# Kernel optimization log

Hardware: AMD Instinct MI355X
Metric: run time of the kernel (lower is better)

## Reference

```python
import jax, jax.numpy as jnp
import numpy as np

N_QUBITS = 14
N_TROTTER = 10
EVO_TIME = 1.0
BATCH = 2048
DIM = 2 ** N_QUBITS

# (-1)**bit_q(idx) for every basis index (Qiskit little-endian: qubit q <-> bit q)
_bits = (np.arange(DIM)[:, None] >> np.arange(N_QUBITS)[None, :]) & 1
_SIGNS = np.asarray(1 - 2 * _bits, dtype=np.float32)  # (DIM, n)


def _apply_1q(psi, U, q, n):
    A = 2 ** (n - 1 - q)
    B = 2 ** q
    psi = psi.reshape(A, 2, B)
    psi = jnp.einsum('ij,ajb->aib', U, psi)
    return psi.reshape(-1)


def _apply_zz(psi, theta, q, n):
    # CX(q,q+1); RZ(theta) on q+1; CX(q,q+1)  ==  diagonal exp(-i*theta/2 * Z_q Z_{q+1})
    A = 2 ** (n - 2 - q)
    B = 2 ** q
    em = jnp.exp(-0.5j * theta)
    ep = jnp.exp(0.5j * theta)
    diag = jnp.stack([em, ep, ep, em])  # axis index = 2*bit_{q+1} + bit_q
    psi = psi.reshape(A, 4, B) * diag[None, :, None]
    return psi.reshape(-1)


def _base_state(J, g):
    # Fixed part of the circuit (same for every sample): H on all qubits, then Trotter steps.
    n = N_QUBITS
    dt = EVO_TIME / N_TROTTER
    inv = 1.0 / np.sqrt(2.0)
    H = jnp.array([[inv, inv], [inv, -inv]], dtype=jnp.complex64)
    psi = jnp.zeros(DIM, dtype=jnp.complex64).at[0].set(1.0)
    for q in range(n):
        psi = _apply_1q(psi, H, q, n)
    for _ in range(N_TROTTER):
        for i in range(n - 1):
            psi = _apply_zz(psi, J[i] * dt, i, n)
        for i in range(n):
            half = 0.5 * g[i] * dt
            c = jnp.cos(half).astype(jnp.complex64)
            ms = -1j * jnp.sin(half)
            RX = jnp.stack([jnp.stack([c, ms]), jnp.stack([ms, c])])
            psi = _apply_1q(psi, RX, i, n)
    return psi


def _expectations(psi):
    # psi: (batch, DIM). Original observable order: block i -> qubit n-1-i, [X, Y, Z].
    n = N_QUBITS
    outs = []
    for i in range(n):
        q = n - 1 - i
        A = 2 ** (n - 1 - q)
        B = 2 ** q
        pr = psi.reshape(-1, A, 2, B)
        p0 = pr[:, :, 0, :]
        p1 = pr[:, :, 1, :]
        c = jnp.sum(jnp.conj(p0) * p1, axis=(1, 2))
        outs.append(2.0 * jnp.real(c))  # <X_q>
        outs.append(2.0 * jnp.imag(c))  # <Y_q>
        outs.append(jnp.sum(p0.real ** 2 + p0.imag ** 2 - p1.real ** 2 - p1.imag ** 2, axis=(1, 2)))  # <Z_q>
    return jnp.stack(outs, axis=1).astype(jnp.float32)


def setup_inputs() -> dict:
    key = jax.random.key(0)
    kx, kj, kg = jax.random.split(key, 3)
    x = jax.random.normal(kx, (BATCH, N_QUBITS), dtype=jnp.float32)
    J = jax.random.uniform(kj, (N_QUBITS - 1,), minval=0.5, maxval=1.5, dtype=jnp.float32)
    g = jax.random.uniform(kg, (N_QUBITS,), minval=0.5, maxval=1.5, dtype=jnp.float32)
    return {"x": x, "J": J, "g": g}


def reference(x, J, g):
    psi0 = _base_state(J, g)  # (DIM,), shared across the batch
    S = jnp.asarray(_SIGNS)   # (DIM, n)
    # Final per-sample RZ(x[b,q]) on qubit q -> diagonal phase exp(-i/2 * sum_q x_q * (-1)^bit_q)
    phase = jnp.exp((-0.5j) * (x @ S.T).astype(jnp.complex64))  # (batch, DIM)
    psi = psi0[None, :] * phase
    return _expectations(psi)
```

## Files before the change

kernel.cpp:

```cpp
#include <hip/hip_runtime.h>

#define NQ     14
#define DIMQ   16384
#define NWG    16
#define NTHR   256

typedef float vfloat4 __attribute__((ext_vector_type(4)));

struct Smem {
    float2 slab[1024];
    float2 tabLo[64];
    float2 tabHi[128];
    float  red[48];
};


__device__ __forceinline__ void ld8v(const float2* p, float rb, float2 r[4]) {
    vfloat4 a, b;
    for (;;) {
        asm volatile("global_load_dwordx4 %0, %2, off sc0 sc1\n\t"
                     "global_load_dwordx4 %1, %2, off offset:16 sc0 sc1\n\t"
                     "s_waitcnt vmcnt(0)"
                     : "=&v"(a), "=&v"(b) : "v"(p) : "memory");
        float m0 = fminf(fminf(a.x * rb, a.y * rb), fminf(a.z * rb, a.w * rb));
        float m1 = fminf(fminf(b.x * rb, b.y * rb), fminf(b.z * rb, b.w * rb));
        bool ok = fminf(m0, m1) > 8.0f;
        if (__ballot(!ok) == 0ull) break;
        __builtin_amdgcn_s_sleep(1);
    }
    r[0] = make_float2(a.x - rb, a.y - rb); r[1] = make_float2(a.z - rb, a.w - rb);
    r[2] = make_float2(b.x - rb, b.y - rb); r[3] = make_float2(b.z - rb, b.w - rb);
}
__device__ __forceinline__ float2 d2f2(double d) { union { double d; float2 f; } u; u.d = d; return u.f; }
__device__ __forceinline__ double f22d(float2 f) { union { double d; float2 f; } u; u.f = f; return u.d; }
__device__ __forceinline__ void st2b(float2* p, float2 v, float wb) {
    float2 e = make_float2(v.x + wb, v.y + wb);
    asm volatile("global_store_dwordx2 %0, %1, off sc0 sc1"
                 : : "v"(p), "v"(f22d(e)) : "memory");
}
__device__ __forceinline__ void st8b(float2* p, const float2 r[4], float wb) {
    vfloat4 a, b;
    a.x = r[0].x + wb; a.y = r[0].y + wb; a.z = r[1].x + wb; a.w = r[1].y + wb;
    b.x = r[2].x + wb; b.y = r[2].y + wb; b.z = r[3].x + wb; b.w = r[3].y + wb;
    asm volatile("global_store_dwordx4 %0, %1, off sc0 sc1\n\t"
                 "global_store_dwordx4 %0, %2, off offset:16 sc0 sc1"
                 : : "v"(p), "v"(a), "v"(b) : "memory");
}
__device__ __forceinline__ void stfb(float* p, float v, float wb) {
    float e = v + wb;
    asm volatile("global_store_dword %0, %1, off sc0 sc1" : : "v"(p), "v"(e) : "memory");
}
__device__ __forceinline__ void ld3v(const float* p, float rb, bool use2,
                                     float& r0, float& r1, float& r2) {
    for (;;) {
        asm volatile("global_load_dword %0, %3, off sc0 sc1\n\t"
                     "global_load_dword %1, %3, off offset:1024 sc0 sc1\n\t"
                     "global_load_dword %2, %3, off offset:2048 sc0 sc1\n\t"
                     "s_waitcnt vmcnt(0)"
                     : "=&v"(r0), "=&v"(r1), "=&v"(r2) : "v"(p) : "memory");
        float m = fminf(r0 * rb, r1 * rb);
        if (use2) m = fminf(m, r2 * rb);
        bool ok = m > 8.0f;
        if (__ballot(!ok) == 0ull) break;
        __builtin_amdgcn_s_sleep(1);
    }
    r0 -= rb; r1 -= rb; r2 -= rb;
}

__device__ __forceinline__ float2 cmulf(float2 a, float2 b) {
    return make_float2(a.x * b.x - a.y * b.y, a.x * b.y + a.y * b.x);
}
__device__ __forceinline__ void bfly(float2& p0, float2& p1, float c, float s) {
    float2 n0 = make_float2(c * p0.x + s * p1.y, c * p0.y - s * p1.x);
    float2 n1 = make_float2(c * p1.x + s * p0.y, c * p1.y - s * p0.x);
    p0 = n0; p1 = n1;
}
__device__ __forceinline__ void bfly_shfl(float2& p, int mask, float c, float s) {
    float qx = __shfl_xor(p.x, mask);
    float qy = __shfl_xor(p.y, mask);
    p = make_float2(c * p.x + s * qy, c * p.y - s * qx);
}
__device__ __forceinline__ void zz_apply(const Smem& sm, float2& a, int k) {
    int d = (k ^ (k >> 1)) & 0x1FFF;
    float2 rot = cmulf(sm.tabLo[d & 63], sm.tabHi[d >> 6]);
    a = cmulf(a, rot);
}
__device__ __forceinline__ void stage_12(float2* slab, float2 r[4], int t) {
    __syncthreads();
#pragma unroll
    for (int j = 0; j < 4; ++j) slab[(t << 2) | j] = r[j];
    __syncthreads();
#pragma unroll
    for (int j = 0; j < 4; ++j) r[j] = slab[t | (j << 8)];
}
__device__ __forceinline__ void stage_21(float2* slab, float2 r[4], int t) {
    __syncthreads();
#pragma unroll
    for (int j = 0; j < 4; ++j) slab[t | (j << 8)] = r[j];
    __syncthreads();
#pragma unroll
    for (int j = 0; j < 4; ++j) r[j] = slab[(t << 2) | j];
}
__device__ __forceinline__ void reduce_qubit(Smem& sm, int sb, int i, int t) {
    float cr = 0.f, ci = 0.f, z = 0.f;
#pragma unroll
    for (int j = 0; j < 4; ++j) {
        const int m = (t << 2) | j;
        const float2 a = sm.slab[m];
        const float n = a.x * a.x + a.y * a.y;
        if ((m >> sb) & 1) {
            z -= n;
        } else {
            z += n;
            const float2 b = sm.slab[m ^ (1 << sb)];
            cr += a.x * b.x + a.y * b.y;
            ci += a.x * b.y - a.y * b.x;
        }
    }
#pragma unroll
    for (int off = 32; off; off >>= 1) {
        cr += __shfl_down(cr, off);
        ci += __shfl_down(ci, off);
        z  += __shfl_down(z, off);
    }
    if ((t & 63) == 0) {
        atomicAdd(&sm.red[3 * i + 0], cr);
        atomicAdd(&sm.red[3 * i + 1], ci);
        atomicAdd(&sm.red[3 * i + 2], z);
    }
}

template <bool FIRST>
__device__ void phaseA(Smem& sm, float2* psi, int w, int t,
                       const float* c, const float* s, float rb, float wb) {
    float2 r[4];
    if (FIRST) {
#pragma unroll
        for (int j = 0; j < 4; ++j) r[j] = make_float2(0.0078125f, 0.0f);
    } else {
        ld8v(&psi[(w << 10) | (t << 2)], rb, r);
#pragma unroll
        for (int b = 2; b < 6; ++b) {
#pragma unroll
            for (int j = 0; j < 4; ++j) bfly_shfl(r[j], 1 << b, c[2 + b], s[2 + b]);
        }
    }
#pragma unroll
    for (int j = 0; j < 4; ++j) zz_apply(sm, r[j], (w << 10) | (t << 2) | j);
    bfly(r[0], r[1], c[0], s[0]); bfly(r[2], r[3], c[0], s[0]);
    bfly(r[0], r[2], c[1], s[1]); bfly(r[1], r[3], c[1], s[1]);
#pragma unroll
    for (int b = 0; b < 6; ++b) {
#pragma unroll
        for (int j = 0; j < 4; ++j) bfly_shfl(r[j], 1 << b, c[2 + b], s[2 + b]);
    }
    stage_12(sm.slab, r, t);
    bfly(r[0], r[1], c[8], s[8]); bfly(r[2], r[3], c[8], s[8]);
    bfly(r[0], r[2], c[9], s[9]); bfly(r[1], r[3], c[9], s[9]);
#pragma unroll
    for (int j = 0; j < 4; ++j) st2b(&psi[(w << 10) | t | (j << 8)], r[j], wb);
}

template <bool KEEPSLAB>
__device__ void phaseB(Smem& sm, float2* psi, int w, int t,
                       const float* c, const float* s, float rb, float wb) {
    float2 r[4];
    const int kbase = ((t >> 2) << 8) | (w << 4) | ((t & 3) << 2);
    ld8v(&psi[kbase], rb, r);
#pragma unroll
    for (int j = 0; j < 4; ++j) bfly_shfl(r[j], 16, c[10], s[10]);
#pragma unroll
    for (int j = 0; j < 4; ++j) bfly_shfl(r[j], 32, c[11], s[11]);
    stage_12(sm.slab, r, t);
    bfly(r[0], r[1], c[12], s[12]); bfly(r[2], r[3], c[12], s[12]);
    bfly(r[0], r[2], c[13], s[13]); bfly(r[1], r[3], c[13], s[13]);
#pragma unroll
    for (int j = 0; j < 4; ++j) {
        const int m = t | (j << 8);
        zz_apply(sm, r[j], ((m >> 4) << 8) | (w << 4) | (m & 15));
    }
    bfly(r[0], r[1], c[12], s[12]); bfly(r[2], r[3], c[12], s[12]);
    bfly(r[0], r[2], c[13], s[13]); bfly(r[1], r[3], c[13], s[13]);
#pragma unroll
    for (int b = 0; b < 4; ++b) {
#pragma unroll
        for (int j = 0; j < 4; ++j) bfly_shfl(r[j], 1 << b, c[b], s[b]);
    }
#pragma unroll
    for (int j = 0; j < 4; ++j) bfly_shfl(r[j], 16, c[8], s[8]);
#pragma unroll
    for (int j = 0; j < 4; ++j) bfly_shfl(r[j], 32, c[9], s[9]);
    stage_21(sm.slab, r, t);
#pragma unroll
    for (int j = 0; j < 4; ++j) bfly_shfl(r[j], 16, c[10], s[10]);
#pragma unroll
    for (int j = 0; j < 4; ++j) bfly_shfl(r[j], 32, c[11], s[11]);
    st8b(&psi[kbase], r, wb);
    if (KEEPSLAB) {
#pragma unroll
        for (int j = 0; j < 4; ++j) sm.slab[(t << 2) | j] = r[j];
    }
}

extern "C" __global__ void __launch_bounds__(NTHR)
qr_all(const float* __restrict__ x, const float* __restrict__ J,
       const float* __restrict__ g, float* __restrict__ out,
       float2* __restrict__ psi, float* __restrict__ P) {
    __shared__ Smem sm;
    const int w = blockIdx.x;
    const int t = threadIdx.x;
    const float dt = 0.1f;

    if (t < 64) {
        float phi = 0.0f;
        for (int i = 0; i < 6; ++i) {
            const float h = 0.5f * J[i] * dt;
            phi += ((t >> i) & 1) ? h : -h;
        }
        float sn, cs; __sincosf(phi, &sn, &cs);
        sm.tabLo[t] = make_float2(cs, sn);
    } else if (t < 192) {
        const int v = t - 64;
        float phi = 0.0f;
        for (int i = 0; i < 7; ++i) {
            const float h = 0.5f * J[6 + i] * dt;
            phi += ((v >> i) & 1) ? h : -h;
        }
        float sn, cs; __sincosf(phi, &sn, &cs);
        sm.tabHi[v] = make_float2(cs, sn);
    }
    if (t < 48) sm.red[t] = 0.0f;
    float cc[NQ], ss[NQ];
#pragma unroll
    for (int i = 0; i < NQ; ++i) __sincosf(0.5f * g[i] * dt, &ss[i], &cc[i]);
    __syncthreads();

    phaseA<true>(sm, psi, w, t, cc, ss, 0.0f, -4.0f);

    float esn[7], ecs[7];
#pragma unroll
    for (int k = 0; k < 7; ++k) {
        const int task = w * NTHR + t + (k << 12);
        const int b = task / NQ;
        const int i = task - b * NQ;
        __sincosf(x[b * NQ + 13 - i], &esn[k], &ecs[k]);
    }

    for (int sstep = 1; sstep <= 9; ++sstep) {
        const float wb = ((sstep + 1) & 1) ? -4.0f : 4.0f;
        const float rb = -wb;
        if (sstep & 1) {
            if (sstep == 9) {
                phaseB<true>(sm, psi, w, t, cc, ss, rb, wb);
                __syncthreads();
#pragma unroll
                for (int q = 0; q <= 3; ++q) reduce_qubit(sm, q, 13 - q, t);
#pragma unroll
                for (int q = 8; q <= 13; ++q) reduce_qubit(sm, q - 4, 13 - q, t);
            } else {
                phaseB<false>(sm, psi, w, t, cc, ss, rb, wb);
            }
        } else {
            phaseA<false>(sm, psi, w, t, cc, ss, rb, wb);
        }
    }

    {
        float2 r[4];
        ld8v(&psi[(w << 10) | (t << 2)], 4.0f, r);
#pragma unroll
        for (int b = 2; b < 6; ++b) {
#pragma unroll
            for (int j = 0; j < 4; ++j) bfly_shfl(r[j], 1 << b, cc[2 + b], ss[2 + b]);
        }
        __syncthreads();
#pragma unroll
        for (int j = 0; j < 4; ++j) sm.slab[(t << 2) | j] = r[j];
        __syncthreads();
#pragma unroll
        for (int q = 4; q <= 7; ++q) reduce_qubit(sm, q, 13 - q, t);
        __syncthreads();
        if (t < 42) stfb(&P[t * NWG + w], sm.red[t], -4.0f);
    }

    float* sumbuf = (float*)sm.slab;
    {
        float r0, r1, r2;
        ld3v(&P[t], -4.0f, t < 160, r0, r1, r2);
        sumbuf[t] = r0; sumbuf[t + 256] = r1; sumbuf[t + 512] = r2;
    }
    __syncthreads();
    float cv = 0.0f;
    if (t < 42) {
#pragma unroll
        for (int k = 0; k < NWG; ++k) cv += sumbuf[t * NWG + k];
    }
    __syncthreads();
    if (t < 42) sm.red[t] = cv;
    __syncthreads();

#pragma unroll
    for (int k = 0; k < 7; ++k) {
        const int task = w * NTHR + t + (k << 12);
        const int b = task / NQ;
        const int i = task - b * NQ;
        const float cr = sm.red[3 * i + 0];
        const float ci = sm.red[3 * i + 1];
        const float zz = sm.red[3 * i + 2];
        const float sn = esn[k], cs = ecs[k];
        float* o = out + b * (3 * NQ) + 3 * i;
        o[0] = 2.0f * (cs * cr - sn * ci);
        o[1] = 2.0f * (sn * cr + cs * ci);
        o[2] = zz;
    }
}

extern "C" void kernel_launch(void* const* d_in, const int* in_sizes, int n_in,
                              void* d_out, int out_size, void* d_ws, size_t ws_size,
                              hipStream_t stream) {
    const float* x = (const float*)d_in[0];
    const float* J = (const float*)d_in[1];
    const float* g = (const float*)d_in[2];
    float* out = (float*)d_out;
    char* ws   = (char*)d_ws;
    float2* psi = (float2*)ws;
    float*  P   = (float*)(ws + DIMQ * sizeof(float2));
    (void)in_sizes; (void)n_in; (void)out_size; (void)ws_size;

    hipLaunchKernelGGL(qr_all, dim3(NWG), dim3(NTHR), 0, stream,
                       x, J, g, out, psi, P);
}
```

Measured before the change: 93.81 us.

## Split state across 64 single-wave workgroups, drop LDS transposes

Changes the launch from 16 workgroups of 256 threads to 64 workgroups of one wavefront each. Each wave now holds 256 amplitudes, so all in-phase butterflies run on registers and cross-lane shuffles, with no LDS slab staging or __syncthreads. Partial expectation values are reduced per wave and written to a workspace with sentinel-biased values. Every wave then polls all 64 partial sets and reduces them by shuffles. This removes LDS round trips and block barriers, at the cost of more workgroups polling global memory at each phase boundary and a larger final gather.

```diff
diff --git a/kernel.cpp b/kernel.cpp
--- a/kernel.cpp
+++ b/kernel.cpp
@@ -1,19 +1,17 @@
 #include <hip/hip_runtime.h>
 
-#define NQ     14
-#define DIMQ   16384
-#define NWG    16
-#define NTHR   256
+#define NQ    14
+#define DIMQ  16384
+#define NWG   64
+#define NTHR  64
 
 typedef float vfloat4 __attribute__((ext_vector_type(4)));
 
 struct Smem {
-    float2 slab[1024];
     float2 tabLo[64];
     float2 tabHi[128];
     float  red[48];
 };
-
 
 __device__ __forceinline__ void ld8v(const float2* p, float rb, float2 r[4]) {
     vfloat4 a, b;
@@ -31,13 +29,6 @@
     r[0] = make_float2(a.x - rb, a.y - rb); r[1] = make_float2(a.z - rb, a.w - rb);
     r[2] = make_float2(b.x - rb, b.y - rb); r[3] = make_float2(b.z - rb, b.w - rb);
 }
-__device__ __forceinline__ float2 d2f2(double d) { union { double d; float2 f; } u; u.d = d; return u.f; }
-__device__ __forceinline__ double f22d(float2 f) { union { double d; float2 f; } u; u.f = f; return u.d; }
-__device__ __forceinline__ void st2b(float2* p, float2 v, float wb) {
-    float2 e = make_float2(v.x + wb, v.y + wb);
-    asm volatile("global_store_dwordx2 %0, %1, off sc0 sc1"
-                 : : "v"(p), "v"(f22d(e)) : "memory");
-}
 __device__ __forceinline__ void st8b(float2* p, const float2 r[4], float wb) {
     vfloat4 a, b;
     a.x = r[0].x + wb; a.y = r[0].y + wb; a.z = r[1].x + wb; a.w = r[1].y + wb;
@@ -50,21 +41,35 @@
     float e = v + wb;
     asm volatile("global_store_dword %0, %1, off sc0 sc1" : : "v"(p), "v"(e) : "memory");
 }
-__device__ __forceinline__ void ld3v(const float* p, float rb, bool use2,
-                                     float& r0, float& r1, float& r2) {
+__device__ __forceinline__ void ld48v(const float* p, vfloat4 v[12]) {
     for (;;) {
-        asm volatile("global_load_dword %0, %3, off sc0 sc1\n\t"
-                     "global_load_dword %1, %3, off offset:1024 sc0 sc1\n\t"
-                     "global_load_dword %2, %3, off offset:2048 sc0 sc1\n\t"
-                     "s_waitcnt vmcnt(0)"
-                     : "=&v"(r0), "=&v"(r1), "=&v"(r2) : "v"(p) : "memory");
-        float m = fminf(r0 * rb, r1 * rb);
-        if (use2) m = fminf(m, r2 * rb);
-        bool ok = m > 8.0f;
+        asm volatile(
+            "global_load_dwordx4 %0,  %12, off sc0 sc1\n\t"
+            "global_load_dwordx4 %1,  %12, off offset:16 sc0 sc1\n\t"
+            "global_load_dwordx4 %2,  %12, off offset:32 sc0 sc1\n\t"
+            "global_load_dwordx4 %3,  %12, off offset:48 sc0 sc1\n\t"
+            "global_load_dwordx4 %4,  %12, off offset:64 sc0 sc1\n\t"
+            "global_load_dwordx4 %5,  %12, off offset:80 sc0 sc1\n\t"
+            "global_load_dwordx4 %6,  %12, off offset:96 sc0 sc1\n\t"
+            "global_load_dwordx4 %7,  %12, off offset:112 sc0 sc1\n\t"
+            "global_load_dwordx4 %8,  %12, off offset:128 sc0 sc1\n\t"
+            "global_load_dwordx4 %9,  %12, off offset:144 sc0 sc1\n\t"
+            "global_load_dwordx4 %10, %12, off offset:160 sc0 sc1\n\t"
+            "global_load_dwordx4 %11, %12, off offset:176 sc0 sc1\n\t"
+            "s_waitcnt vmcnt(0)"
+            : "=&v"(v[0]), "=&v"(v[1]), "=&v"(v[2]), "=&v"(v[3]),
+              "=&v"(v[4]), "=&v"(v[5]), "=&v"(v[6]), "=&v"(v[7]),
+              "=&v"(v[8]), "=&v"(v[9]), "=&v"(v[10]), "=&v"(v[11])
+            : "v"(p) : "memory");
+        float mx = -1e30f;
+#pragma unroll
+        for (int k = 0; k < 10; ++k)
+            mx = fmaxf(mx, fmaxf(fmaxf(v[k].x, v[k].y), fmaxf(v[k].z, v[k].w)));
+        mx = fmaxf(mx, fmaxf(v[10].x, v[10].y));
+        bool ok = mx < -2.0f;
         if (__ballot(!ok) == 0ull) break;
         __builtin_amdgcn_s_sleep(1);
     }
-    r0 -= rb; r1 -= rb; r2 -= rb;
 }
 
 __device__ __forceinline__ float2 cmulf(float2 a, float2 b) {
@@ -85,120 +90,102 @@
     float2 rot = cmulf(sm.tabLo[d & 63], sm.tabHi[d >> 6]);
     a = cmulf(a, rot);
 }
-__device__ __forceinline__ void stage_12(float2* slab, float2 r[4], int t) {
-    __syncthreads();
-#pragma unroll
-    for (int j = 0; j < 4; ++j) slab[(t << 2) | j] = r[j];
-    __syncthreads();
-#pragma unroll
-    for (int j = 0; j < 4; ++j) r[j] = slab[t | (j << 8)];
-}
-__device__ __forceinline__ void stage_21(float2* slab, float2 r[4], int t) {
-    __syncthreads();
-#pragma unroll
-    for (int j = 0; j < 4; ++j) slab[t | (j << 8)] = r[j];
-    __syncthreads();
-#pragma unroll
-    for (int j = 0; j < 4; ++j) r[j] = slab[(t << 2) | j];
-}
-__device__ __forceinline__ void reduce_qubit(Smem& sm, int sb, int i, int t) {
-    float cr = 0.f, ci = 0.f, z = 0.f;
-#pragma unroll
-    for (int j = 0; j < 4; ++j) {
-        const int m = (t << 2) | j;
-        const float2 a = sm.slab[m];
-        const float n = a.x * a.x + a.y * a.y;
-        if ((m >> sb) & 1) {
-            z -= n;
-        } else {
-            z += n;
-            const float2 b = sm.slab[m ^ (1 << sb)];
-            cr += a.x * b.x + a.y * b.y;
-            ci += a.x * b.y - a.y * b.x;
-        }
-    }
+__device__ __forceinline__ void rx_reg01(float2 r[4], const float* c, const float* s) {
+    bfly(r[0], r[1], c[0], s[0]); bfly(r[2], r[3], c[0], s[0]);
+    bfly(r[0], r[2], c[1], s[1]); bfly(r[1], r[3], c[1], s[1]);
+}
+
+__device__ __forceinline__ void wave_store_triple(float cr, float ci, float z,
+                                                  float* P, int wg, int i) {
 #pragma unroll
     for (int off = 32; off; off >>= 1) {
         cr += __shfl_down(cr, off);
         ci += __shfl_down(ci, off);
         z  += __shfl_down(z, off);
     }
-    if ((t & 63) == 0) {
-        atomicAdd(&sm.red[3 * i + 0], cr);
-        atomicAdd(&sm.red[3 * i + 1], ci);
-        atomicAdd(&sm.red[3 * i + 2], z);
-    }
+    if (threadIdx.x == 0) {
+        stfb(&P[wg * 48 + 3 * i + 0], cr, -4.0f);
+        stfb(&P[wg * 48 + 3 * i + 1], ci, -4.0f);
+        stfb(&P[wg * 48 + 3 * i + 2], z,  -4.0f);
+    }
+}
+__device__ __forceinline__ void reduce_lane_qubit(const float2 r[4], int b,
+                                                  float* P, int wg, int i, int t) {
+    const int bit = (t >> b) & 1;
+    const float sel = bit ? 0.0f : 1.0f;
+    float cr = 0.f, ci = 0.f, z = 0.f;
+#pragma unroll
+    for (int j = 0; j < 4; ++j) {
+        const float px = __shfl_xor(r[j].x, 1 << b);
+        const float py = __shfl_xor(r[j].y, 1 << b);
+        const float n  = r[j].x * r[j].x + r[j].y * r[j].y;
+        cr += sel * (r[j].x * px + r[j].y * py);
+        ci += sel * (r[j].x * py - r[j].y * px);
+        z  += bit ? -n : n;
+    }
+    wave_store_triple(cr, ci, z, P, wg, i);
 }
 
 template <bool FIRST>
-__device__ void phaseA(Smem& sm, float2* psi, int w, int t,
+__device__ void phaseA(const Smem& sm, float2* psi, int base,
                        const float* c, const float* s, float rb, float wb) {
     float2 r[4];
     if (FIRST) {
 #pragma unroll
         for (int j = 0; j < 4; ++j) r[j] = make_float2(0.0078125f, 0.0f);
     } else {
-        ld8v(&psi[(w << 10) | (t << 2)], rb, r);
-#pragma unroll
-        for (int b = 2; b < 6; ++b) {
+        ld8v(&psi[base], rb, r);
+#pragma unroll
+        for (int b = 0; b < 6; ++b)
 #pragma unroll
             for (int j = 0; j < 4; ++j) bfly_shfl(r[j], 1 << b, c[2 + b], s[2 + b]);
-        }
-    }
-#pragma unroll
-    for (int j = 0; j < 4; ++j) zz_apply(sm, r[j], (w << 10) | (t << 2) | j);
-    bfly(r[0], r[1], c[0], s[0]); bfly(r[2], r[3], c[0], s[0]);
-    bfly(r[0], r[2], c[1], s[1]); bfly(r[1], r[3], c[1], s[1]);
-#pragma unroll
-    for (int b = 0; b < 6; ++b) {
+    }
+#pragma unroll
+    for (int j = 0; j < 4; ++j) zz_apply(sm, r[j], base | j);
+#pragma unroll
+    for (int b = 0; b < 6; ++b)
 #pragma unroll
         for (int j = 0; j < 4; ++j) bfly_shfl(r[j], 1 << b, c[2 + b], s[2 + b]);
-    }
-    stage_12(sm.slab, r, t);
-    bfly(r[0], r[1], c[8], s[8]); bfly(r[2], r[3], c[8], s[8]);
-    bfly(r[0], r[2], c[9], s[9]); bfly(r[1], r[3], c[9], s[9]);
-#pragma unroll
-    for (int j = 0; j < 4; ++j) st2b(&psi[(w << 10) | t | (j << 8)], r[j], wb);
-}
-
-template <bool KEEPSLAB>
-__device__ void phaseB(Smem& sm, float2* psi, int w, int t,
-                       const float* c, const float* s, float rb, float wb) {
+    st8b(&psi[base], r, wb);
+}
+
+template <bool REDUCE>
+__device__ void phaseB(const Smem& sm, float2* psi, float* P, int base,
+                       int wg, int t, const float* c, const float* s,
+                       float rb, float wb) {
     float2 r[4];
-    const int kbase = ((t >> 2) << 8) | (w << 4) | ((t & 3) << 2);
-    ld8v(&psi[kbase], rb, r);
-#pragma unroll
-    for (int j = 0; j < 4; ++j) bfly_shfl(r[j], 16, c[10], s[10]);
-#pragma unroll
-    for (int j = 0; j < 4; ++j) bfly_shfl(r[j], 32, c[11], s[11]);
-    stage_12(sm.slab, r, t);
-    bfly(r[0], r[1], c[12], s[12]); bfly(r[2], r[3], c[12], s[12]);
-    bfly(r[0], r[2], c[13], s[13]); bfly(r[1], r[3], c[13], s[13]);
-#pragma unroll
-    for (int j = 0; j < 4; ++j) {
-        const int m = t | (j << 8);
-        zz_apply(sm, r[j], ((m >> 4) << 8) | (w << 4) | (m & 15));
-    }
-    bfly(r[0], r[1], c[12], s[12]); bfly(r[2], r[3], c[12], s[12]);
-    bfly(r[0], r[2], c[13], s[13]); bfly(r[1], r[3], c[13], s[13]);
-#pragma unroll
-    for (int b = 0; b < 4; ++b) {
-#pragma unroll
-        for (int j = 0; j < 4; ++j) bfly_shfl(r[j], 1 << b, c[b], s[b]);
-    }
-#pragma unroll
-    for (int j = 0; j < 4; ++j) bfly_shfl(r[j], 16, c[8], s[8]);
-#pragma unroll
-    for (int j = 0; j < 4; ++j) bfly_shfl(r[j], 32, c[9], s[9]);
-    stage_21(sm.slab, r, t);
-#pragma unroll
-    for (int j = 0; j < 4; ++j) bfly_shfl(r[j], 16, c[10], s[10]);
-#pragma unroll
-    for (int j = 0; j < 4; ++j) bfly_shfl(r[j], 32, c[11], s[11]);
-    st8b(&psi[kbase], r, wb);
-    if (KEEPSLAB) {
-#pragma unroll
-        for (int j = 0; j < 4; ++j) sm.slab[(t << 2) | j] = r[j];
+    ld8v(&psi[base], rb, r);
+    rx_reg01(r, c, s);
+#pragma unroll
+    for (int b = 0; b < 6; ++b)
+#pragma unroll
+        for (int j = 0; j < 4; ++j) bfly_shfl(r[j], 1 << b, c[8 + b], s[8 + b]);
+#pragma unroll
+    for (int j = 0; j < 4; ++j) zz_apply(sm, r[j], base | j);
+    rx_reg01(r, c, s);
+#pragma unroll
+    for (int b = 0; b < 6; ++b)
+#pragma unroll
+        for (int j = 0; j < 4; ++j) bfly_shfl(r[j], 1 << b, c[8 + b], s[8 + b]);
+    st8b(&psi[base], r, wb);
+
+    if (REDUCE) {
+        {
+            float cr = r[0].x*r[1].x + r[0].y*r[1].y + r[2].x*r[3].x + r[2].y*r[3].y;
+            float ci = r[0].x*r[1].y - r[0].y*r[1].x + r[2].x*r[3].y - r[2].y*r[3].x;
+            float z  = (r[0].x*r[0].x + r[0].y*r[0].y + r[2].x*r[2].x + r[2].y*r[2].y)
+                     - (r[1].x*r[1].x + r[1].y*r[1].y + r[3].x*r[3].x + r[3].y*r[3].y);
+            wave_store_triple(cr, ci, z, P, wg, 13);
+        }
+        {
+            float cr = r[0].x*r[2].x + r[0].y*r[2].y + r[1].x*r[3].x + r[1].y*r[3].y;
+            float ci = r[0].x*r[2].y - r[0].y*r[2].x + r[1].x*r[3].y - r[1].y*r[3].x;
+            float z  = (r[0].x*r[0].x + r[0].y*r[0].y + r[1].x*r[1].x + r[1].y*r[1].y)
+                     - (r[2].x*r[2].x + r[2].y*r[2].y + r[3].x*r[3].x + r[3].y*r[3].y);
+            wave_store_triple(cr, ci, z, P, wg, 12);
+        }
+#pragma unroll
+        for (int b = 0; b < 6; ++b) reduce_lane_qubit(r, b, P, wg, 5 - b, t);
     }
 }
 
@@ -207,21 +194,23 @@
        const float* __restrict__ g, float* __restrict__ out,
        float2* __restrict__ psi, float* __restrict__ P) {
     __shared__ Smem sm;
-    const int w = blockIdx.x;
-    const int t = threadIdx.x;
+    const int wg = blockIdx.x;
+    const int t  = threadIdx.x;
     const float dt = 0.1f;
 
-    if (t < 64) {
-        float phi = 0.0f;
+    {
+        float phi = 0.f;
         for (int i = 0; i < 6; ++i) {
             const float h = 0.5f * J[i] * dt;
             phi += ((t >> i) & 1) ? h : -h;
         }
         float sn, cs; __sincosf(phi, &sn, &cs);
         sm.tabLo[t] = make_float2(cs, sn);
-    } else if (t < 192) {
-        const int v = t - 64;
-        float phi = 0.0f;
+    }
+#pragma unroll
+    for (int rep = 0; rep < 2; ++rep) {
+        const int v = t + (rep << 6);
+        float phi = 0.f;
         for (int i = 0; i < 7; ++i) {
             const float h = 0.5f * J[6 + i] * dt;
             phi += ((v >> i) & 1) ? h : -h;
@@ -229,88 +218,70 @@
         float sn, cs; __sincosf(phi, &sn, &cs);
         sm.tabHi[v] = make_float2(cs, sn);
     }
-    if (t < 48) sm.red[t] = 0.0f;
     float cc[NQ], ss[NQ];
 #pragma unroll
     for (int i = 0; i < NQ; ++i) __sincosf(0.5f * g[i] * dt, &ss[i], &cc[i]);
     __syncthreads();
 
-    phaseA<true>(sm, psi, w, t, cc, ss, 0.0f, -4.0f);
+    const int aBase = (wg << 8) | (t << 2);
+    const int bBase = (t << 8) | (wg << 2);
+
+    phaseA<true>(sm, psi, aBase, cc, ss, 0.f, -4.f);
 
     float esn[7], ecs[7];
 #pragma unroll
     for (int k = 0; k < 7; ++k) {
-        const int task = w * NTHR + t + (k << 12);
+        const int task = (wg << 6) | t | (k << 12);
         const int b = task / NQ;
         const int i = task - b * NQ;
         __sincosf(x[b * NQ + 13 - i], &esn[k], &ecs[k]);
     }
 
-    for (int sstep = 1; sstep <= 9; ++sstep) {
-        const float wb = ((sstep + 1) & 1) ? -4.0f : 4.0f;
+#pragma unroll 1
+    for (int p = 2; p <= 10; ++p) {
+        const float wb = (p & 1) ? -4.f : 4.f;
         const float rb = -wb;
-        if (sstep & 1) {
-            if (sstep == 9) {
-                phaseB<true>(sm, psi, w, t, cc, ss, rb, wb);
-                __syncthreads();
-#pragma unroll
-                for (int q = 0; q <= 3; ++q) reduce_qubit(sm, q, 13 - q, t);
-#pragma unroll
-                for (int q = 8; q <= 13; ++q) reduce_qubit(sm, q - 4, 13 - q, t);
-            } else {
-                phaseB<false>(sm, psi, w, t, cc, ss, rb, wb);
-            }
+        if (p & 1) {
+            phaseA<false>(sm, psi, aBase, cc, ss, rb, wb);
+        } else if (p == 10) {
+            phaseB<true >(sm, psi, P, bBase, wg, t, cc, ss, rb, wb);
         } else {
-            phaseA<false>(sm, psi, w, t, cc, ss, rb, wb);
+            phaseB<false>(sm, psi, P, bBase, wg, t, cc, ss, rb, wb);
         }
     }
 
     {
         float2 r[4];
-        ld8v(&psi[(w << 10) | (t << 2)], 4.0f, r);
-#pragma unroll
-        for (int b = 2; b < 6; ++b) {
+        ld8v(&psi[aBase], 4.0f, r);
+#pragma unroll
+        for (int b = 0; b < 6; ++b)
 #pragma unroll
             for (int j = 0; j < 4; ++j) bfly_shfl(r[j], 1 << b, cc[2 + b], ss[2 + b]);
-        }
-        __syncthreads();
-#pragma unroll
-        for (int j = 0; j < 4; ++j) sm.slab[(t << 2) | j] = r[j];
-        __syncthreads();
-#pragma unroll
-        for (int q = 4; q <= 7; ++q) reduce_qubit(sm, q, 13 - q, t);
-        __syncthreads();
-        if (t < 42) stfb(&P[t * NWG + w], sm.red[t], -4.0f);
-    }
-
-    float* sumbuf = (float*)sm.slab;
-    {
-        float r0, r1, r2;
-        ld3v(&P[t], -4.0f, t < 160, r0, r1, r2);
-        sumbuf[t] = r0; sumbuf[t + 256] = r1; sumbuf[t + 512] = r2;
+#pragma unroll
+        for (int b = 0; b < 6; ++b) reduce_lane_qubit(r, b, P, wg, 11 - b, t);
+    }
+
+    vfloat4 v[12];
+    ld48v(&P[t * 48], v);
+#pragma unroll
+    for (int e = 0; e < 42; ++e) {
+        float sv = v[e >> 2][e & 3] + 4.0f;
+#pragma unroll
+        for (int off = 32; off; off >>= 1) sv += __shfl_down(sv, off);
+        if (t == 0) sm.red[e] = sv;
     }
     __syncthreads();
-    float cv = 0.0f;
-    if (t < 42) {
-#pragma unroll
-        for (int k = 0; k < NWG; ++k) cv += sumbuf[t * NWG + k];
-    }
-    __syncthreads();
-    if (t < 42) sm.red[t] = cv;
-    __syncthreads();
-
 #pragma unroll
     for (int k = 0; k < 7; ++k) {
-        const int task = w * NTHR + t + (k << 12);
+        const int task = (wg << 6) | t | (k << 12);
         const int b = task / NQ;
         const int i = task - b * NQ;
         const float cr = sm.red[3 * i + 0];
         const float ci = sm.red[3 * i + 1];
         const float zz = sm.red[3 * i + 2];
-        const float sn = esn[k], cs = ecs[k];
         float* o = out + b * (3 * NQ) + 3 * i;
-        o[0] = 2.0f * (cs * cr - sn * ci);
-        o[1] = 2.0f * (sn * cr + cs * ci);
+        o[0] = 2.0f * (ecs[k] * cr - esn[k] * ci);
+        o[1] = 2.0f * (esn[k] * cr + ecs[k] * ci);
         o[2] = zz;
     }
 }
```

Measured after the change: 98.17 us. 4.7% more time.
